# Kernel optimization log

Hardware: AMD Instinct MI355X
Metric: run time of the kernel (lower is better)

## Reference

```python
import jax, jax.numpy as jnp
import numpy as np

B, IN, H = 8192, 1024, 1024

def setup_inputs() -> dict:
    key = jax.random.key(0)
    ks = jax.random.split(key, 12)
    s_i = 1.0 / np.sqrt(IN)   # lecun-normal-ish scale for input kernels
    s_h = 1.0 / np.sqrt(H)
    d = {
        'inputs': jax.random.normal(ks[0], (B, IN), jnp.float32),
        'c': jax.random.normal(ks[1], (B, H), jnp.float32),
        'h': jax.random.normal(ks[2], (B, H), jnp.float32),
    }
    for n, k in zip(['Wii', 'Wif', 'Wig', 'Wio'], ks[3:7]):
        d[n] = jax.random.normal(k, (IN, H), jnp.float32) * s_i
    for n, k in zip(['Whi', 'Whf', 'Whg', 'Who'], ks[7:11]):
        d[n] = jax.random.normal(k, (H, H), jnp.float32) * s_h
    for n in ['bi', 'bf', 'bg', 'bo']:
        d[n] = jnp.zeros((H,), jnp.float32)
    return d

def reference(inputs, c, h, Wii, Wif, Wig, Wio, Whi, Whf, Whg, Who, bi, bf, bg, bo):
    # i = sigmoid(x Wii + h Whi + bi); f, o likewise; g = tanh(x Wig + h Whg + bg)
    i = jax.nn.sigmoid(inputs @ Wii + h @ Whi + bi)
    f = jax.nn.sigmoid(inputs @ Wif + h @ Whf + bf)
    g = jnp.tanh(inputs @ Wig + h @ Whg + bg)
    o = jax.nn.sigmoid(inputs @ Wio + h @ Who + bo)
    new_c = f * c + i * g
    new_h = o * jnp.tanh(new_c)
    return (new_c, new_h)
```

## Files before the change

kernel.cpp:

```cpp
#include <hip/hip_runtime.h>
#include <hip/hip_bf16.h>
#include <cstdint>


#define B_DIM 8192
#define H_DIM 1024
#define K2    2048
#define N4    4096
#define BK    64
#define BM    128
#define BN    256

typedef __bf16 bf16x8 __attribute__((ext_vector_type(8)));
typedef __bf16 bf16x4 __attribute__((ext_vector_type(4)));
typedef float  f32x4  __attribute__((ext_vector_type(4)));
typedef float  f32x16 __attribute__((ext_vector_type(16)));

__device__ __forceinline__ void async_load16(const __bf16* g, __bf16* l) {
  __builtin_amdgcn_global_load_lds(
      (__attribute__((address_space(1))) void*)(g),
      (__attribute__((address_space(3))) void*)(l),
      16, 0, 0);
}

__device__ __forceinline__ float sigm(float x) {
  return 1.0f / (1.0f + __expf(-x));
}
__device__ __forceinline__ float tanh_fast(float x) {
  return 2.0f / (1.0f + __expf(-2.0f * x)) - 1.0f;
}

__global__ void cast_a(const float* __restrict__ x, const float* __restrict__ h,
                       __bf16* __restrict__ A) {
  int row = blockIdx.x;
  int k = threadIdx.x << 3;
  const float* src = (k < H_DIM) ? (x + (size_t)row * H_DIM + k)
                                 : (h + (size_t)row * H_DIM + (k - H_DIM));
  float4 v0 = *(const float4*)src;
  float4 v1 = *(const float4*)(src + 4);
  bf16x8 o;
  o[0] = (__bf16)v0.x; o[1] = (__bf16)v0.y; o[2] = (__bf16)v0.z; o[3] = (__bf16)v0.w;
  o[4] = (__bf16)v1.x; o[5] = (__bf16)v1.y; o[6] = (__bf16)v1.z; o[7] = (__bf16)v1.w;
  *(bf16x8*)&A[(size_t)row * K2 + k] = o;
}

__global__ void cast_w(const float* __restrict__ Wii, const float* __restrict__ Wif,
                       const float* __restrict__ Wig, const float* __restrict__ Wio,
                       const float* __restrict__ Whi, const float* __restrict__ Whf,
                       const float* __restrict__ Whg, const float* __restrict__ Who,
                       __bf16* __restrict__ Bt) {
  __shared__ float tile[64][33];
  int k0 = blockIdx.x * 64;
  int j0 = blockIdx.y * 32;
  int gate = blockIdx.z;
  const float* Wi[4] = {Wii, Wif, Wig, Wio};
  const float* Wh[4] = {Whi, Whf, Whg, Who};
  const float* W = (k0 < H_DIM) ? Wi[gate] : Wh[gate];
  int kb = (k0 < H_DIM) ? k0 : (k0 - H_DIM);

  int col = threadIdx.x & 31;
  int rr  = threadIdx.x >> 5;
#pragma unroll
  for (int p = 0; p < 8; ++p)
    tile[p * 8 + rr][col] = W[(size_t)(kb + p * 8 + rr) * H_DIM + j0 + col];
  __syncthreads();

  int jj = threadIdx.x >> 3;
  int ko = threadIdx.x & 7;
  int j = j0 + jj;
  int p = ((j >> 5) << 7) + (gate << 5) + (j & 31);
  bf16x8 o;
#pragma unroll
  for (int t = 0; t < 8; ++t) o[t] = (__bf16)tile[ko * 8 + t][jj];
  *(bf16x8*)&Bt[(size_t)p * K2 + k0 + ko * 8] = o;
}

__global__ __launch_bounds__(256, 2) void lstm_gemm(
    const __bf16* __restrict__ A,
    const __bf16* __restrict__ Bt,
    const float* __restrict__ c,
    const float* __restrict__ bi, const float* __restrict__ bf_,
    const float* __restrict__ bg, const float* __restrict__ bo,
    float* __restrict__ out_c, float* __restrict__ out_h) {
  __shared__ __align__(16) __bf16 As[BM * BK];
  __shared__ __align__(16) __bf16 Bs[BN * BK];

  const int tid  = threadIdx.x;
  const int wave = tid >> 6;
  const int lane = tid & 63;
  const int wm   = wave >> 1;
  const int wn   = wave & 1;
  const int m0   = blockIdx.x * BM;
  const int n0   = blockIdx.y * BN;

  f32x16 acc[2][4] = {};

  const int l31 = lane & 31;
  const int h8  = lane >> 5;

  const int rin  = lane >> 3;
  const int slot = lane & 7;
  const int sg   = slot ^ rin;
  const __bf16* gA[4]; const __bf16* gB[8];
  __bf16* lA[4]; __bf16* lB[8];
#pragma unroll
  for (int cc = 0; cc < 4; ++cc) {
    int r = wave * 32 + cc * 8 + rin;
    gA[cc] = A + (size_t)(m0 + r) * K2 + sg * 8;
    lA[cc] = &As[(wave * 4 + cc) * 512];
  }
#pragma unroll
  for (int cc = 0; cc < 8; ++cc) {
    int r = wave * 64 + cc * 8 + rin;
    gB[cc] = Bt + (size_t)(n0 + r) * K2 + sg * 8;
    lB[cc] = &Bs[(wave * 8 + cc) * 512];
  }

  for (int k0 = 0; k0 < K2; k0 += BK) {
    __syncthreads();
#pragma unroll
    for (int cc = 0; cc < 4; ++cc) async_load16(gA[cc] + k0, lA[cc]);
#pragma unroll
    for (int cc = 0; cc < 8; ++cc) async_load16(gB[cc] + k0, lB[cc]);
    __syncthreads();

#pragma unroll
    for (int ks = 0; ks < 4; ++ks) {
      bf16x8 af[2], bfr[4];
      const int sw = ((ks * 2 + h8) ^ (l31 & 7)) * 8;
#pragma unroll
      for (int t = 0; t < 2; ++t)
        af[t] = *(const bf16x8*)&As[(wm * 64 + t * 32 + l31) * BK + sw];
#pragma unroll
      for (int t = 0; t < 4; ++t)
        bfr[t] = *(const bf16x8*)&Bs[(wn * 128 + t * 32 + l31) * BK + sw];

#pragma unroll
      for (int tm = 0; tm < 2; ++tm)
#pragma unroll
        for (int tn = 0; tn < 4; ++tn)
          acc[tm][tn] = __builtin_amdgcn_mfma_f32_32x32x16_bf16(
              af[tm], bfr[tn], acc[tm][tn], 0, 0, 0);
    }
  }

  const int j = blockIdx.y * 64 + wn * 32 + l31;
  const float vbi = bi[j], vbf = bf_[j], vbg = bg[j], vbo = bo[j];

#pragma unroll
  for (int tm = 0; tm < 2; ++tm) {
#pragma unroll
    for (int r = 0; r < 16; ++r) {
      int row = m0 + wm * 64 + tm * 32 + 4 * h8 + (r & 3) + 8 * (r >> 2);
      float gi = sigm(acc[tm][0][r] + vbi);
      float gf = sigm(acc[tm][1][r] + vbf);
      float gg = tanh_fast(acc[tm][2][r] + vbg);
      float go = sigm(acc[tm][3][r] + vbo);
      size_t idx = (size_t)row * H_DIM + j;
      float cv = c[idx];
      float nc = gf * cv + gi * gg;
      float nh = go * tanh_fast(nc);
      out_c[idx] = nc;
      out_h[idx] = nh;
    }
  }
}

extern "C" void kernel_launch(void* const* d_in, const int* in_sizes, int n_in,
                              void* d_out, int out_size, void* d_ws, size_t ws_size,
                              hipStream_t stream) {
  const float* x   = (const float*)d_in[0];
  const float* c   = (const float*)d_in[1];
  const float* h   = (const float*)d_in[2];
  const float* Wii = (const float*)d_in[3];
  const float* Wif = (const float*)d_in[4];
  const float* Wig = (const float*)d_in[5];
  const float* Wio = (const float*)d_in[6];
  const float* Whi = (const float*)d_in[7];
  const float* Whf = (const float*)d_in[8];
  const float* Whg = (const float*)d_in[9];
  const float* Who = (const float*)d_in[10];
  const float* bi  = (const float*)d_in[11];
  const float* bf_ = (const float*)d_in[12];
  const float* bg  = (const float*)d_in[13];
  const float* bo  = (const float*)d_in[14];

  __bf16* Abf = (__bf16*)d_ws;
  __bf16* Bt  = (__bf16*)((char*)d_ws + (size_t)B_DIM * K2 * 2);

  float* out_c = (float*)d_out;
  float* out_h = out_c + (size_t)B_DIM * H_DIM;

  cast_a<<<B_DIM, 256, 0, stream>>>(x, h, Abf);
  dim3 gw(K2 / 64, H_DIM / 32, 4);
  cast_w<<<gw, 256, 0, stream>>>(Wii, Wif, Wig, Wio, Whi, Whf, Whg, Who, Bt);
  dim3 gg(B_DIM / BM, N4 / BN);
  lstm_gemm<<<gg, 256, 0, stream>>>(Abf, Bt, c, bi, bf_, bg, bo, out_c, out_h);
}
```

Baseline: 345.2 us.

## Rewrite LSTM GEMM as 256x256 double-buffered pipelined kernel with 16x16 MFMA

Grows the GEMM tile to 256x256 with 8 waves per block and switches to 16x16x32 bf16 MFMAs. The K loop becomes a double-buffered LDS pipeline with explicit vmcnt gates, split barriers and raised MFMA priority, so global loads overlap with compute. The weight interleave layout changes to 16-column gate groups, and blocks are remapped with a swizzle for L2 locality. The aim is to hide load latency and raise MFMA utilisation, at the cost of heavier register pressure and fragile hand-placed waitcnt ordering.

```diff
diff --git a/kernel.cpp b/kernel.cpp
--- a/kernel.cpp
+++ b/kernel.cpp
@@ -8,13 +8,12 @@
 #define K2    2048
 #define N4    4096
 #define BK    64
-#define BM    128
+#define BM    256
 #define BN    256
+#define NT    (K2 / BK)
 
 typedef __bf16 bf16x8 __attribute__((ext_vector_type(8)));
-typedef __bf16 bf16x4 __attribute__((ext_vector_type(4)));
 typedef float  f32x4  __attribute__((ext_vector_type(4)));
-typedef float  f32x16 __attribute__((ext_vector_type(16)));
 
 __device__ __forceinline__ void async_load16(const __bf16* g, __bf16* l) {
   __builtin_amdgcn_global_load_lds(
@@ -68,100 +67,151 @@
   int jj = threadIdx.x >> 3;
   int ko = threadIdx.x & 7;
   int j = j0 + jj;
-  int p = ((j >> 5) << 7) + (gate << 5) + (j & 31);
+  int p = ((j >> 4) << 6) + (gate << 4) + (j & 15);
   bf16x8 o;
 #pragma unroll
   for (int t = 0; t < 8; ++t) o[t] = (__bf16)tile[ko * 8 + t][jj];
   *(bf16x8*)&Bt[(size_t)p * K2 + k0 + ko * 8] = o;
 }
 
-__global__ __launch_bounds__(256, 2) void lstm_gemm(
+
+#define STAGE_A(D, KH, TT) do { \
+    async_load16(gA0 + (size_t)(TT) * 64 + (KH) * 32, &As_s[D][KH][wave << 9]); \
+    async_load16(gA1 + (size_t)(TT) * 64 + (KH) * 32, &As_s[D][KH][4096 + (wave << 9)]); \
+  } while (0)
+#define STAGE_B(D, KH, TT) do { \
+    async_load16(gB0 + (size_t)(TT) * 64 + (KH) * 32, &Bs_s[D][KH][wave << 9]); \
+    async_load16(gB1 + (size_t)(TT) * 64 + (KH) * 32, &Bs_s[D][KH][4096 + (wave << 9)]); \
+  } while (0)
+
+#define LOADA(D, KK, MH) do { \
+    const __bf16* ap_ = &As_s[D][KK][(wm << 12) + ((MH) << 11) + lane_part]; \
+    aF[0] = *(const bf16x8*)(ap_); \
+    aF[1] = *(const bf16x8*)(ap_ + 512); \
+    aF[2] = *(const bf16x8*)(ap_ + 1024); \
+    aF[3] = *(const bf16x8*)(ap_ + 1536); \
+  } while (0)
+#define LOADB(D, KK) do { \
+    const __bf16* bp_ = &Bs_s[D][KK][(wn << 11) + lane_part]; \
+    bF[0] = *(const bf16x8*)(bp_); \
+    bF[1] = *(const bf16x8*)(bp_ + 512); \
+    bF[2] = *(const bf16x8*)(bp_ + 1024); \
+    bF[3] = *(const bf16x8*)(bp_ + 1536); \
+  } while (0)
+
+#define BARW() do { \
+    __builtin_amdgcn_s_barrier(); \
+    asm volatile("s_waitcnt lgkmcnt(0)" ::: "memory"); \
+    __builtin_amdgcn_sched_barrier(0); \
+  } while (0)
+#define ENDBAR() __builtin_amdgcn_s_barrier()
+#define GATE8() asm volatile("s_waitcnt vmcnt(8)" ::: "memory")
+#define GATE4() asm volatile("s_waitcnt vmcnt(4)" ::: "memory")
+#define GATE0() asm volatile("s_waitcnt vmcnt(0)" ::: "memory")
+
+#define MFMA_Q(MH) do { \
+    __builtin_amdgcn_s_setprio(1); \
+    _Pragma("unroll") \
+    for (int i2 = 0; i2 < 4; ++i2) { \
+      _Pragma("unroll") \
+      for (int n2 = 0; n2 < 4; ++n2) \
+        acc[(MH) * 4 + i2][n2] = __builtin_amdgcn_mfma_f32_16x16x32_bf16( \
+            aF[i2], bF[n2], acc[(MH) * 4 + i2][n2], 0, 0, 0); \
+    } \
+    __builtin_amdgcn_s_setprio(0); \
+  } while (0)
+
+__global__ __launch_bounds__(512, 2) void lstm_gemm(
     const __bf16* __restrict__ A,
     const __bf16* __restrict__ Bt,
     const float* __restrict__ c,
     const float* __restrict__ bi, const float* __restrict__ bf_,
     const float* __restrict__ bg, const float* __restrict__ bo,
     float* __restrict__ out_c, float* __restrict__ out_h) {
-  __shared__ __align__(16) __bf16 As[BM * BK];
-  __shared__ __align__(16) __bf16 Bs[BN * BK];
+  __shared__ __align__(16) __bf16 As_s[2][2][256 * 32];
+  __shared__ __align__(16) __bf16 Bs_s[2][2][256 * 32];
+
+  const int wg  = blockIdx.x;
+  const int swz = ((wg & 7) << 6) + (wg >> 3);
+  const int bx = swz & 31;
+  const int by = swz >> 5;
+  const int m0 = bx << 8;
+  const int n0 = by << 8;
 
   const int tid  = threadIdx.x;
   const int wave = tid >> 6;
   const int lane = tid & 63;
-  const int wm   = wave >> 1;
-  const int wn   = wave & 1;
-  const int m0   = blockIdx.x * BM;
-  const int n0   = blockIdx.y * BN;
-
-  f32x16 acc[2][4] = {};
-
-  const int l31 = lane & 31;
-  const int h8  = lane >> 5;
-
-  const int rin  = lane >> 3;
-  const int slot = lane & 7;
-  const int sg   = slot ^ rin;
-  const __bf16* gA[4]; const __bf16* gB[8];
-  __bf16* lA[4]; __bf16* lB[8];
-#pragma unroll
-  for (int cc = 0; cc < 4; ++cc) {
-    int r = wave * 32 + cc * 8 + rin;
-    gA[cc] = A + (size_t)(m0 + r) * K2 + sg * 8;
-    lA[cc] = &As[(wave * 4 + cc) * 512];
-  }
-#pragma unroll
-  for (int cc = 0; cc < 8; ++cc) {
-    int r = wave * 64 + cc * 8 + rin;
-    gB[cc] = Bt + (size_t)(n0 + r) * K2 + sg * 8;
-    lB[cc] = &Bs[(wave * 8 + cc) * 512];
-  }
-
-  for (int k0 = 0; k0 < K2; k0 += BK) {
-    __syncthreads();
-#pragma unroll
-    for (int cc = 0; cc < 4; ++cc) async_load16(gA[cc] + k0, lA[cc]);
-#pragma unroll
-    for (int cc = 0; cc < 8; ++cc) async_load16(gB[cc] + k0, lB[cc]);
-    __syncthreads();
-
-#pragma unroll
-    for (int ks = 0; ks < 4; ++ks) {
-      bf16x8 af[2], bfr[4];
-      const int sw = ((ks * 2 + h8) ^ (l31 & 7)) * 8;
-#pragma unroll
-      for (int t = 0; t < 2; ++t)
-        af[t] = *(const bf16x8*)&As[(wm * 64 + t * 32 + l31) * BK + sw];
-#pragma unroll
-      for (int t = 0; t < 4; ++t)
-        bfr[t] = *(const bf16x8*)&Bs[(wn * 128 + t * 32 + l31) * BK + sw];
-
-#pragma unroll
-      for (int tm = 0; tm < 2; ++tm)
-#pragma unroll
-        for (int tn = 0; tn < 4; ++tn)
-          acc[tm][tn] = __builtin_amdgcn_mfma_f32_32x32x16_bf16(
-              af[tm], bfr[tn], acc[tm][tn], 0, 0, 0);
-    }
-  }
-
-  const int j = blockIdx.y * 64 + wn * 32 + l31;
-  const float vbi = bi[j], vbf = bf_[j], vbg = bg[j], vbo = bo[j];
-
-#pragma unroll
-  for (int tm = 0; tm < 2; ++tm) {
-#pragma unroll
-    for (int r = 0; r < 16; ++r) {
-      int row = m0 + wm * 64 + tm * 32 + 4 * h8 + (r & 3) + 8 * (r >> 2);
-      float gi = sigm(acc[tm][0][r] + vbi);
-      float gf = sigm(acc[tm][1][r] + vbf);
-      float gg = tanh_fast(acc[tm][2][r] + vbg);
-      float go = sigm(acc[tm][3][r] + vbo);
-      size_t idx = (size_t)row * H_DIM + j;
-      float cv = c[idx];
-      float nc = gf * cv + gi * gg;
-      float nh = go * tanh_fast(nc);
+  const int wm   = wave >> 2;
+  const int wn   = wave & 3;
+
+  const int srow = (wave << 4) + (lane >> 2);
+  const int sgc  = (lane & 3) ^ ((lane >> 3) & 3);
+  const __bf16* gA0 = A  + (size_t)(m0 + srow) * K2 + sgc * 8;
+  const __bf16* gA1 = gA0 + (size_t)128 * K2;
+  const __bf16* gB0 = Bt + (size_t)(n0 + srow) * K2 + sgc * 8;
+  const __bf16* gB1 = gB0 + (size_t)128 * K2;
+
+  const int lane_part = ((lane & 15) << 5) + ((((lane >> 4) ^ ((lane >> 1) & 3))) << 3);
+
+  f32x4 acc[8][4] = {};
+  bf16x8 aF[4], bF[4];
+
+  STAGE_A(0, 0, 0); STAGE_B(0, 0, 0);
+  STAGE_A(0, 1, 0); STAGE_B(0, 1, 0);
+  STAGE_A(1, 0, 1); STAGE_B(1, 0, 1);
+  GATE8();
+  __builtin_amdgcn_s_barrier();
+
+  for (int t = 0; t < NT - 2; ++t) {
+    const int db = t & 1;
+    LOADA(db, 0, 0); LOADB(db, 0); STAGE_A(db ^ 1, 1, t + 1);
+    BARW(); MFMA_Q(0); ENDBAR();
+    LOADA(db, 0, 1); STAGE_B(db ^ 1, 1, t + 1);
+    BARW(); MFMA_Q(1); GATE8(); ENDBAR();
+    LOADA(db, 1, 0); LOADB(db, 1); STAGE_A(db, 0, t + 2);
+    BARW(); MFMA_Q(0); ENDBAR();
+    LOADA(db, 1, 1); STAGE_B(db, 0, t + 2);
+    BARW(); MFMA_Q(1); GATE8(); ENDBAR();
+  }
+
+  {
+    LOADA(0, 0, 0); LOADB(0, 0); STAGE_A(1, 1, NT - 1);
+    BARW(); MFMA_Q(0); ENDBAR();
+    LOADA(0, 0, 1); STAGE_B(1, 1, NT - 1);
+    BARW(); MFMA_Q(1); GATE8(); ENDBAR();
+    LOADA(0, 1, 0); LOADB(0, 1);
+    BARW(); MFMA_Q(0); ENDBAR();
+    LOADA(0, 1, 1);
+    BARW(); MFMA_Q(1); GATE4(); ENDBAR();
+  }
+  {
+    LOADA(1, 0, 0); LOADB(1, 0);
+    BARW(); MFMA_Q(0); ENDBAR();
+    LOADA(1, 0, 1);
+    BARW(); MFMA_Q(1); GATE0(); ENDBAR();
+    LOADA(1, 1, 0); LOADB(1, 1);
+    BARW(); MFMA_Q(0); ENDBAR();
+    LOADA(1, 1, 1);
+    BARW(); MFMA_Q(1);
+  }
+
+  const int jj = (by << 6) + (wn << 4) + (lane & 15);
+  const float vbi = bi[jj], vbf = bf_[jj], vbg = bg[jj], vbo = bo[jj];
+  const int row_base = m0 + (wm << 7) + ((lane >> 4) << 2);
+#pragma unroll
+  for (int mi = 0; mi < 8; ++mi) {
+#pragma unroll
+    for (int r = 0; r < 4; ++r) {
+      const int row = row_base + mi * 16 + r;
+      const size_t idx = (size_t)row * H_DIM + jj;
+      const float gi = sigm(acc[mi][0][r] + vbi);
+      const float gf = sigm(acc[mi][1][r] + vbf);
+      const float gg = tanh_fast(acc[mi][2][r] + vbg);
+      const float go = sigm(acc[mi][3][r] + vbo);
+      const float cv = c[idx];
+      const float nc = gf * cv + gi * gg;
       out_c[idx] = nc;
-      out_h[idx] = nh;
+      out_h[idx] = go * tanh_fast(nc);
     }
   }
 }
@@ -194,6 +244,6 @@
   cast_a<<<B_DIM, 256, 0, stream>>>(x, h, Abf);
   dim3 gw(K2 / 64, H_DIM / 32, 4);
   cast_w<<<gw, 256, 0, stream>>>(Wii, Wif, Wig, Wio, Whi, Whf, Whg, Who, Bt);
-  dim3 gg(B_DIM / BM, N4 / BN);
-  lstm_gemm<<<gg, 256, 0, stream>>>(Abf, Bt, c, bi, bf_, bg, bo, out_c, out_h);
-}
+  lstm_gemm<<<dim3((B_DIM / BM) * (N4 / BN)), 512, 0, stream>>>(
+      Abf, Bt, c, bi, bf_, bg, bo, out_c, out_h);
+}
```

Measured after the change: 360.8 us. 1.05x slower.
